# Kernel optimization log

Hardware: AMD Instinct MI355X
Metric: run time of the kernel (lower is better)

Reference implementation:

```python
import jax, jax.numpy as jnp
import numpy as np
from jax import lax

B, CI, CO, H, W = 32, 64, 64, 128, 128
NUM_EXPERTS = 5
NUM_TASKS = 10  # num_tasks=9 + 1 internal global task
K = 5


def setup_inputs() -> dict:
    key = jax.random.key(0)
    ks = jax.random.split(key, 9)
    # kaiming_uniform_ with a=sqrt(5), fan_out -> bound = sqrt(6/((1+5)*fan_out))
    def kaiming(k, co, ci, ksz):
        fan_out = co * ksz * ksz
        bound = np.sqrt(6.0 / (6.0 * fan_out))
        return jax.random.uniform(k, (co, ci, ksz, ksz), jnp.float32, -bound, bound)
    gw_bound = 1.0 / np.sqrt(NUM_TASKS)
    return {
        "x": jax.random.normal(ks[0], (B, CI, H, W), jnp.float32),
        "task_id": jax.random.randint(ks[1], (B,), 0, NUM_TASKS),
        "gate_w": jax.random.uniform(ks[2], (NUM_EXPERTS * CO, NUM_TASKS), jnp.float32, -gw_bound, gw_bound),
        "gate_b": jax.random.uniform(ks[3], (NUM_EXPERTS * CO,), jnp.float32, -gw_bound, gw_bound),
        "w5": kaiming(ks[4], CO, CI, 5),
        "w3": kaiming(ks[5], CO, CI, 3),
        "w1": kaiming(ks[6], CO, CI, 1),
        "wavg3": kaiming(ks[7], CO, CI, 1),
        "wavg5": kaiming(ks[8], CO, CI, 1),
    }


def _expert_bank(w5, w3, w1, wavg3, wavg5):
    # All experts expressed as 5x5 kernels, stacked: [E, O, I, 5, 5]
    pad = lambda w, p: jnp.pad(w, ((0, 0), (0, 0), (p, p), (p, p)))
    avg3 = jnp.full((3, 3), 1.0 / 9.0, w5.dtype)
    avg5 = jnp.full((5, 5), 1.0 / 25.0, w5.dtype)
    e_conv5 = w5
    e_conv3 = pad(w3, 1)
    e_conv1 = pad(w1, 2)
    e_avg3 = pad(wavg3 * avg3[None, None], 1)  # [O,I,1,1]*[3,3] broadcast
    e_avg5 = wavg5 * avg5[None, None]
    return jnp.stack([e_conv5, e_conv3, e_conv1, e_avg3, e_avg5])


def reference(x, task_id, gate_w, gate_b, w5, w3, w1, wavg3, wavg5):
    # Gate: one-hot task -> per-(expert, out_channel) routing weights
    t = jax.nn.one_hot(task_id, NUM_TASKS, dtype=x.dtype)          # [B, T]
    g = t @ gate_w.T + gate_b                                       # [B, E*O]
    g = jax.nn.softmax(g.reshape(-1, NUM_EXPERTS, CO), axis=1)      # [B, E, O]

    experts = _expert_bank(w5, w3, w1, wavg3, wavg5)                # [E, O, I, 5, 5]
    # Batched kernel synthesis (replaces per-sample python loop of einsums)
    w = jnp.einsum('eoikl,beo->boikl', experts, g)                  # [B, O, I, 5, 5]

    # Per-sample conv2d, stride 1, 'same' padding
    def conv1(xi, wi):
        return lax.conv_general_dilated(
            xi[None], wi, (1, 1), 'SAME',
            dimension_numbers=('NCHW', 'OIHW', 'NCHW'))[0]
    y = jax.vmap(conv1)(x, w)                                       # [B, O, H, W]
    # conv_type='final' -> Identity subsequent layer; eval mode -> task_id unchanged
    return y, task_id
```

## Files before the change

### kernel.cpp

```cpp
#include <hip/hip_runtime.h>


using bf16x8   = __attribute__((ext_vector_type(8)))  __bf16;
using floatx16 = __attribute__((ext_vector_type(16))) float;

#define WK_OFFSET_BYTES 69206016ull

static __device__ __forceinline__ unsigned short f2bf(float f) {
    unsigned int u = __float_as_uint(f);
    u += 0x7FFFu + ((u >> 16) & 1u);
    return (unsigned short)(u >> 16);
}

static __device__ __forceinline__ floatx16 mfma16(bf16x8 a, bf16x8 b, floatx16 c) {
    return __builtin_amdgcn_mfma_f32_32x32x16_bf16(a, b, c, 0, 0, 0);
}

__global__ __launch_bounds__(256) void prep_kernel(
    const float* __restrict__ gate_w, const float* __restrict__ gate_b,
    const float* __restrict__ w5, const float* __restrict__ w3,
    const float* __restrict__ w1, const float* __restrict__ wavg3,
    const float* __restrict__ wavg5, const int* __restrict__ task_id,
    unsigned short* __restrict__ wk, float* __restrict__ out_task)
{
    const int t = blockIdx.x >> 4;
    const int chunk = blockIdx.x & 15;
    const int tid = threadIdx.x;

    __shared__ float g[5][64];
    if (tid < 64) {
        float l[5];
        float m = -1e30f;
        #pragma unroll
        for (int e = 0; e < 5; ++e) {
            l[e] = gate_w[(e * 64 + tid) * 10 + t] + gate_b[e * 64 + tid];
            m = fmaxf(m, l[e]);
        }
        float s = 0.f;
        #pragma unroll
        for (int e = 0; e < 5; ++e) { l[e] = expf(l[e] - m); s += l[e]; }
        float inv = 1.f / s;
        #pragma unroll
        for (int e = 0; e < 5; ++e) g[e][tid] = l[e] * inv;
    }
    __syncthreads();

    for (int it = 0; it < 25; ++it) {
        int idx = chunk * 6400 + it * 256 + tid;
        int ci  = idx & 63;
        int o   = (idx >> 6) & 63;
        int tap = idx >> 12;
        int ky = tap / 5, kx = tap - ky * 5;

        float v = g[0][o] * w5[(o * 64 + ci) * 25 + tap];
        bool in3 = (ky >= 1 && ky <= 3 && kx >= 1 && kx <= 3);
        if (in3) {
            v += g[1][o] * w3[(o * 64 + ci) * 9 + (ky - 1) * 3 + (kx - 1)];
            v += g[3][o] * wavg3[o * 64 + ci] * (1.f / 9.f);
        }
        if (ky == 2 && kx == 2) v += g[2][o] * w1[o * 64 + ci];
        v += g[4][o] * wavg5[o * 64 + ci] * (1.f / 25.f);

        wk[(t * 25 + tap) * 4096 + o * 64 + ci] = f2bf(v);
    }

    if (blockIdx.x == 0 && tid < 32) out_task[tid] = (float)task_id[tid];
}

__global__ __launch_bounds__(256) void transform_kernel(
    const float* __restrict__ x, unsigned short* __restrict__ xt)
{
    const int bh = blockIdx.x;
    const int b = bh >> 7, h = bh & 127;

    for (int i = threadIdx.x; i < 1056; i += 256) {
        int cc = i / 132;
        int wp = i - cc * 132;
        unsigned int pk[4] = {0u, 0u, 0u, 0u};
        if (wp >= 2 && wp < 130) {
            int w = wp - 2;
            const float* xp = x + (((b * 64 + cc * 8) * 128 + h) * 128 + w);
            #pragma unroll
            for (int j = 0; j < 4; ++j) {
                unsigned short lo = f2bf(xp[(2 * j)     * 16384]);
                unsigned short hi = f2bf(xp[(2 * j + 1) * 16384]);
                pk[j] = (unsigned int)lo | ((unsigned int)hi << 16);
            }
        }
        uint4* dst = (uint4*)(xt + (size_t)bh * 8448 + (size_t)i * 8);
        *dst = make_uint4(pk[0], pk[1], pk[2], pk[3]);
    }
}

__global__ __launch_bounds__(256, 2) void conv_kernel(
    const unsigned short* __restrict__ xt, const unsigned short* __restrict__ wk,
    const int* __restrict__ task_id, float* __restrict__ out)
{
    __shared__ unsigned short lds[16896];

    const int blk = blockIdx.x;
    const int b  = blk >> 5;
    const int ht = blk & 31;
    const int h0 = ht * 4;
    const int t  = task_id[b];

    const int tid  = threadIdx.x;
    const int lane = tid & 63;
    const int wave = tid >> 6;
    const int lane31 = lane & 31;
    const int laneh  = lane >> 5;

    floatx16 acc[2][4];
    #pragma unroll
    for (int c = 0; c < 2; ++c)
        #pragma unroll
        for (int p = 0; p < 4; ++p)
            #pragma unroll
            for (int r = 0; r < 16; ++r) acc[c][p][r] = 0.f;

    const unsigned short* wkt = wk + t * 102400;
    const size_t xrow = (size_t)(b * 128) * 8448;

    for (int q = 0; q < 4; ++q) {
        __syncthreads();
        for (int i = tid; i < 2112; i += 256) {
            int r = i / 264;
            int rem = i - r * 264;
            int h = h0 - 2 + r;
            uint4 v = make_uint4(0u, 0u, 0u, 0u);
            if (h >= 0 && h < 128)
                v = *(const uint4*)(xt + xrow + (size_t)h * 8448
                                       + (size_t)q * 2112 + (size_t)rem * 8);
            *(uint4*)(lds + i * 8) = v;
        }
        __syncthreads();

        for (int ky = 0; ky < 5; ++ky) {
            const unsigned short* lrow = lds + (wave + ky) * 2112 + laneh * 1056;
            const unsigned short* wrow = wkt + (ky * 5) * 4096 + q * 16 + laneh * 8;
            #pragma unroll
            for (int kx = 0; kx < 5; ++kx) {
                const unsigned short* ap = wrow + kx * 4096;
                bf16x8 a0 = *(const bf16x8*)(ap + lane31 * 64);
                bf16x8 a1 = *(const bf16x8*)(ap + (lane31 + 32) * 64);

                bf16x8 bb[4];
                #pragma unroll
                for (int p = 0; p < 4; ++p)
                    bb[p] = *(const bf16x8*)(lrow + (p * 32 + lane31 + kx) * 8);

                #pragma unroll
                for (int p = 0; p < 4; ++p) {
                    acc[0][p] = mfma16(a0, bb[p], acc[0][p]);
                    acc[1][p] = mfma16(a1, bb[p], acc[1][p]);
                }
            }
        }
    }

    const int h = h0 + wave;
    #pragma unroll
    for (int c = 0; c < 2; ++c) {
        #pragma unroll
        for (int p = 0; p < 4; ++p) {
            int w = p * 32 + lane31;
            #pragma unroll
            for (int reg = 0; reg < 16; ++reg) {
                int co = c * 32 + (reg & 3) + 8 * (reg >> 2) + 4 * laneh;
                out[((size_t)(b * 64 + co) * 128 + h) * 128 + w] = acc[c][p][reg];
            }
        }
    }
}

extern "C" void kernel_launch(void* const* d_in, const int* in_sizes, int n_in,
                              void* d_out, int out_size, void* d_ws, size_t ws_size,
                              hipStream_t stream) {
    const float* x       = (const float*)d_in[0];
    const int*   task_id = (const int*)  d_in[1];
    const float* gate_w  = (const float*)d_in[2];
    const float* gate_b  = (const float*)d_in[3];
    const float* w5      = (const float*)d_in[4];
    const float* w3      = (const float*)d_in[5];
    const float* w1      = (const float*)d_in[6];
    const float* wavg3   = (const float*)d_in[7];
    const float* wavg5   = (const float*)d_in[8];

    float* out = (float*)d_out;
    float* out_task = out + 32 * 64 * 128 * 128;

    unsigned short* xt = (unsigned short*)d_ws;
    unsigned short* wk = (unsigned short*)((char*)d_ws + WK_OFFSET_BYTES);

    prep_kernel<<<dim3(160), dim3(256), 0, stream>>>(
        gate_w, gate_b, w5, w3, w1, wavg3, wavg5, task_id, wk, out_task);
    transform_kernel<<<dim3(32 * 128), dim3(256), 0, stream>>>(x, xt);
    conv_kernel<<<dim3(32 * 32), dim3(256), 0, stream>>>(xt, wk, task_id, out);
}
```

Before: 413.9 us.

## Double-buffer conv inputs via direct global-to-LDS loads and stage weights in LDS

The prep and transform kernels merge into one launch. The transformed input is now stored with two zero-padded halo rows per image, so the conv kernel needs no bounds checks. The conv kernel uses 512-thread blocks that each cover 8 output rows. It double-buffers input channel chunks in LDS with async global_load_lds and stages the per-task weights in LDS instead of reading them from global memory on every tap. The block index is also remapped and wave priority is raised around the MFMA loop. This trades more LDS per block (about 150KB) and extra barriers for fewer global weight loads and load/compute overlap, and occupancy may fall.

Measured after the change: 351.9 us. 1.18x faster.

```diff
diff --git a/kernel.cpp b/kernel.cpp
--- a/kernel.cpp
+++ b/kernel.cpp
@@ -1,10 +1,9 @@
 #include <hip/hip_runtime.h>
 
+#define WK_OFFSET_BYTES 71368704ull
 
 using bf16x8   = __attribute__((ext_vector_type(8)))  __bf16;
 using floatx16 = __attribute__((ext_vector_type(16))) float;
-
-#define WK_OFFSET_BYTES 69206016ull
 
 static __device__ __forceinline__ unsigned short f2bf(float f) {
     unsigned int u = __float_as_uint(f);
@@ -16,92 +15,102 @@
     return __builtin_amdgcn_mfma_f32_32x32x16_bf16(a, b, c, 0, 0, 0);
 }
 
-__global__ __launch_bounds__(256) void prep_kernel(
+static __device__ __forceinline__ void gload_lds16(const void* g, void* l) {
+    __builtin_amdgcn_global_load_lds(
+        (const __attribute__((address_space(1))) void*)g,
+        (__attribute__((address_space(3))) void*)l, 16, 0, 0);
+}
+
+__global__ __launch_bounds__(256) void pre_kernel(
+    const float* __restrict__ x,
     const float* __restrict__ gate_w, const float* __restrict__ gate_b,
     const float* __restrict__ w5, const float* __restrict__ w3,
     const float* __restrict__ w1, const float* __restrict__ wavg3,
     const float* __restrict__ wavg5, const int* __restrict__ task_id,
-    unsigned short* __restrict__ wk, float* __restrict__ out_task)
+    unsigned short* __restrict__ xt, unsigned short* __restrict__ wk,
+    float* __restrict__ out_task)
 {
-    const int t = blockIdx.x >> 4;
-    const int chunk = blockIdx.x & 15;
+    const int blk = blockIdx.x;
     const int tid = threadIdx.x;
-
     __shared__ float g[5][64];
-    if (tid < 64) {
-        float l[5];
-        float m = -1e30f;
-        #pragma unroll
-        for (int e = 0; e < 5; ++e) {
-            l[e] = gate_w[(e * 64 + tid) * 10 + t] + gate_b[e * 64 + tid];
-            m = fmaxf(m, l[e]);
-        }
-        float s = 0.f;
-        #pragma unroll
-        for (int e = 0; e < 5; ++e) { l[e] = expf(l[e] - m); s += l[e]; }
-        float inv = 1.f / s;
-        #pragma unroll
-        for (int e = 0; e < 5; ++e) g[e][tid] = l[e] * inv;
+
+    if (blk < 4224) {
+        const int b  = blk / 132;
+        const int hp = blk - b * 132;
+        const int h  = hp - 2;
+        const bool vrow = (h >= 0) && (h < 128);
+        unsigned short* dst_row = xt + (size_t)blk * 8448;
+
+        for (int i = tid; i < 1056; i += 256) {
+            int cc = i / 132;
+            int wp = i - cc * 132;
+            unsigned int pk[4] = {0u, 0u, 0u, 0u};
+            if (vrow && wp >= 2 && wp < 130) {
+                const float* xp = x + (((size_t)(b * 64 + cc * 8) * 128 + h) * 128 + (wp - 2));
+                #pragma unroll
+                for (int j = 0; j < 4; ++j) {
+                    unsigned short lo = f2bf(xp[(2 * j)     * 16384]);
+                    unsigned short hi = f2bf(xp[(2 * j + 1) * 16384]);
+                    pk[j] = (unsigned int)lo | ((unsigned int)hi << 16);
+                }
+            }
+            *(uint4*)(dst_row + (size_t)i * 8) = make_uint4(pk[0], pk[1], pk[2], pk[3]);
+        }
+    } else {
+        const int pb = blk - 4224;
+        const int t = pb >> 4;
+        const int chunk = pb & 15;
+
+        if (tid < 64) {
+            float l[5];
+            float m = -1e30f;
+            #pragma unroll
+            for (int e = 0; e < 5; ++e) {
+                l[e] = gate_w[(e * 64 + tid) * 10 + t] + gate_b[e * 64 + tid];
+                m = fmaxf(m, l[e]);
+            }
+            float s = 0.f;
+            #pragma unroll
+            for (int e = 0; e < 5; ++e) { l[e] = expf(l[e] - m); s += l[e]; }
+            float inv = 1.f / s;
+            #pragma unroll
+            for (int e = 0; e < 5; ++e) g[e][tid] = l[e] * inv;
+        }
+        __syncthreads();
+
+        for (int it = 0; it < 25; ++it) {
+            int idx = chunk * 6400 + it * 256 + tid;
+            int ci  = idx & 63;
+            int o   = (idx >> 6) & 63;
+            int tap = idx >> 12;
+            int ky = tap / 5, kx = tap - ky * 5;
+
+            float v = g[0][o] * w5[(o * 64 + ci) * 25 + tap];
+            bool in3 = (ky >= 1 && ky <= 3 && kx >= 1 && kx <= 3);
+            if (in3) {
+                v += g[1][o] * w3[(o * 64 + ci) * 9 + (ky - 1) * 3 + (kx - 1)];
+                v += g[3][o] * wavg3[o * 64 + ci] * (1.f / 9.f);
+            }
+            if (ky == 2 && kx == 2) v += g[2][o] * w1[o * 64 + ci];
+            v += g[4][o] * wavg5[o * 64 + ci] * (1.f / 25.f);
+
+            wk[(t * 25 + tap) * 4096 + o * 64 + ci] = f2bf(v);
+        }
+
+        if (pb == 0 && tid < 32) out_task[tid] = (float)task_id[tid];
     }
-    __syncthreads();
-
-    for (int it = 0; it < 25; ++it) {
-        int idx = chunk * 6400 + it * 256 + tid;
-        int ci  = idx & 63;
-        int o   = (idx >> 6) & 63;
-        int tap = idx >> 12;
-        int ky = tap / 5, kx = tap - ky * 5;
-
-        float v = g[0][o] * w5[(o * 64 + ci) * 25 + tap];
-        bool in3 = (ky >= 1 && ky <= 3 && kx >= 1 && kx <= 3);
-        if (in3) {
-            v += g[1][o] * w3[(o * 64 + ci) * 9 + (ky - 1) * 3 + (kx - 1)];
-            v += g[3][o] * wavg3[o * 64 + ci] * (1.f / 9.f);
-        }
-        if (ky == 2 && kx == 2) v += g[2][o] * w1[o * 64 + ci];
-        v += g[4][o] * wavg5[o * 64 + ci] * (1.f / 25.f);
-
-        wk[(t * 25 + tap) * 4096 + o * 64 + ci] = f2bf(v);
-    }
-
-    if (blockIdx.x == 0 && tid < 32) out_task[tid] = (float)task_id[tid];
-}
-
-__global__ __launch_bounds__(256) void transform_kernel(
-    const float* __restrict__ x, unsigned short* __restrict__ xt)
-{
-    const int bh = blockIdx.x;
-    const int b = bh >> 7, h = bh & 127;
-
-    for (int i = threadIdx.x; i < 1056; i += 256) {
-        int cc = i / 132;
-        int wp = i - cc * 132;
-        unsigned int pk[4] = {0u, 0u, 0u, 0u};
-        if (wp >= 2 && wp < 130) {
-            int w = wp - 2;
-            const float* xp = x + (((b * 64 + cc * 8) * 128 + h) * 128 + w);
-            #pragma unroll
-            for (int j = 0; j < 4; ++j) {
-                unsigned short lo = f2bf(xp[(2 * j)     * 16384]);
-                unsigned short hi = f2bf(xp[(2 * j + 1) * 16384]);
-                pk[j] = (unsigned int)lo | ((unsigned int)hi << 16);
-            }
-        }
-        uint4* dst = (uint4*)(xt + (size_t)bh * 8448 + (size_t)i * 8);
-        *dst = make_uint4(pk[0], pk[1], pk[2], pk[3]);
-    }
-}
-
-__global__ __launch_bounds__(256, 2) void conv_kernel(
+}
+
+__global__ __launch_bounds__(512, 2) void conv_kernel(
     const unsigned short* __restrict__ xt, const unsigned short* __restrict__ wk,
     const int* __restrict__ task_id, float* __restrict__ out)
 {
-    __shared__ unsigned short lds[16896];
-
-    const int blk = blockIdx.x;
-    const int b  = blk >> 5;
-    const int ht = blk & 31;
-    const int h0 = ht * 4;
+    __shared__ unsigned short ibuf[2][25344];
+    __shared__ unsigned short wlds[25600];
+
+    const int blk = ((blockIdx.x & 7) << 6) | (blockIdx.x >> 3);
+    const int b  = blk >> 4;
+    const int ht = blk & 15;
     const int t  = task_id[b];
 
     const int tid  = threadIdx.x;
@@ -119,30 +128,68 @@
             for (int r = 0; r < 16; ++r) acc[c][p][r] = 0.f;
 
     const unsigned short* wkt = wk + t * 102400;
-    const size_t xrow = (size_t)(b * 128) * 8448;
-
-    for (int q = 0; q < 4; ++q) {
-        __syncthreads();
-        for (int i = tid; i < 2112; i += 256) {
+    const size_t ibase0 = ((size_t)(b * 132 + ht * 8)) * 8448;
+
+    auto stage_i = [&](int s, int q) {
+        const unsigned short* gsrc = xt + ibase0 + q * 2112;
+        unsigned short* ldst = &ibuf[s][0];
+        #pragma unroll
+        for (int j = 0; j < 6; ++j) {
+            int i = j * 512 + tid;
             int r = i / 264;
             int rem = i - r * 264;
-            int h = h0 - 2 + r;
-            uint4 v = make_uint4(0u, 0u, 0u, 0u);
-            if (h >= 0 && h < 128)
-                v = *(const uint4*)(xt + xrow + (size_t)h * 8448
-                                       + (size_t)q * 2112 + (size_t)rem * 8);
-            *(uint4*)(lds + i * 8) = v;
-        }
-        __syncthreads();
-
+            gload_lds16(gsrc + (size_t)r * 8448 + rem * 8, ldst + i * 8);
+        }
+        if (tid < 96) {
+            int i = 3072 + tid;
+            int r = i / 264;
+            int rem = i - r * 264;
+            gload_lds16(gsrc + (size_t)r * 8448 + rem * 8, ldst + i * 8);
+        }
+    };
+    auto stage_w = [&](int q) {
+        const unsigned short* gsrc = wkt + q * 16;
+        unsigned short* ldst = &wlds[0];
+        #pragma unroll
+        for (int j = 0; j < 6; ++j) {
+            int i = j * 512 + tid;
+            int tap = i >> 7;
+            int rem = i & 127;
+            int cih = rem >> 6;
+            int co  = rem & 63;
+            gload_lds16(gsrc + tap * 4096 + co * 64 + cih * 8, ldst + i * 8);
+        }
+        if (tid < 128) {
+            int i = 3072 + tid;
+            int tap = i >> 7;
+            int rem = i & 127;
+            int cih = rem >> 6;
+            int co  = rem & 63;
+            gload_lds16(gsrc + tap * 4096 + co * 64 + cih * 8, ldst + i * 8);
+        }
+    };
+
+    stage_w(0);
+    stage_i(0, 0);
+    asm volatile("s_waitcnt vmcnt(0)" ::: "memory");
+    __builtin_amdgcn_s_barrier();
+    __builtin_amdgcn_sched_barrier(0);
+
+    for (int q = 0; q < 4; ++q) {
+        const int s = q & 1;
+        if (q < 3) stage_i(s ^ 1, q + 1);
+
+        const unsigned short* ib = &ibuf[s][0];
+        __builtin_amdgcn_s_setprio(1);
+        #pragma unroll
         for (int ky = 0; ky < 5; ++ky) {
-            const unsigned short* lrow = lds + (wave + ky) * 2112 + laneh * 1056;
-            const unsigned short* wrow = wkt + (ky * 5) * 4096 + q * 16 + laneh * 8;
+            const unsigned short* lrow = ib + (wave + ky) * 2112 + laneh * 1056;
+            const unsigned short* wrow = wlds + (ky * 5) * 1024 + laneh * 512 + lane31 * 8;
             #pragma unroll
             for (int kx = 0; kx < 5; ++kx) {
-                const unsigned short* ap = wrow + kx * 4096;
-                bf16x8 a0 = *(const bf16x8*)(ap + lane31 * 64);
-                bf16x8 a1 = *(const bf16x8*)(ap + (lane31 + 32) * 64);
+                const unsigned short* ap = wrow + kx * 1024;
+                bf16x8 a0 = *(const bf16x8*)(ap);
+                bf16x8 a1 = *(const bf16x8*)(ap + 256);
 
                 bf16x8 bb[4];
                 #pragma unroll
@@ -156,9 +203,20 @@
                 }
             }
         }
+        __builtin_amdgcn_s_setprio(0);
+
+        asm volatile("s_waitcnt lgkmcnt(0)" ::: "memory");
+        __builtin_amdgcn_s_barrier();
+        __builtin_amdgcn_sched_barrier(0);
+        if (q < 3) {
+            stage_w(q + 1);
+            asm volatile("s_waitcnt vmcnt(0)" ::: "memory");
+            __builtin_amdgcn_s_barrier();
+            __builtin_amdgcn_sched_barrier(0);
+        }
     }
 
-    const int h = h0 + wave;
+    const int h = ht * 8 + wave;
     #pragma unroll
     for (int c = 0; c < 2; ++c) {
         #pragma unroll
@@ -192,8 +250,7 @@
     unsigned short* xt = (unsigned short*)d_ws;
     unsigned short* wk = (unsigned short*)((char*)d_ws + WK_OFFSET_BYTES);
 
-    prep_kernel<<<dim3(160), dim3(256), 0, stream>>>(
-        gate_w, gate_b, w5, w3, w1, wavg3, wavg5, task_id, wk, out_task);
-    transform_kernel<<<dim3(32 * 128), dim3(256), 0, stream>>>(x, xt);
-    conv_kernel<<<dim3(32 * 32), dim3(256), 0, stream>>>(xt, wk, task_id, out);
-}
+    pre_kernel<<<dim3(4384), dim3(256), 0, stream>>>(
+        x, gate_w, gate_b, w5, w3, w1, wavg3, wavg5, task_id, xt, wk, out_task);
+    conv_kernel<<<dim3(512), dim3(512), 0, stream>>>(xt, wk, task_id, out);
+}
```
